# Kernel tuning notes

Hardware: AMD Instinct MI355X
Metric: run time of the kernel (lower is better)

The kernel has to match this reference:

```python
import jax, jax.numpy as jnp
import numpy as np

B, S, D, F, E = 2, 2048, 1024, 4096, 8

def _xavier(key, shape):
    fan_in, fan_out = shape[-2], shape[-1]
    lim = np.sqrt(6.0 / (fan_in + fan_out))
    return jax.random.uniform(key, shape, jnp.float32, -lim, lim)

def setup_inputs() -> dict:
    key = jax.random.key(0)
    kx, k1, k2, kg = jax.random.split(key, 4)
    return {
        "x": jax.random.normal(kx, (B, S, D), jnp.float32),
        "W1": _xavier(k1, (E, D, F)),            # expert linear1 weights
        "b1": jnp.zeros((E, F), jnp.float32),
        "W2": _xavier(k2, (E, F, D)),            # expert linear2 weights
        "b2": jnp.zeros((E, D), jnp.float32),
        "Wg": _xavier(kg, (D, E)),               # gate weight
        "bg": jnp.zeros((E,), jnp.float32),
        "num_experts_per_token": 2,
    }

def reference(x, W1, b1, W2, b2, Wg, bg, num_experts_per_token):
    k = num_experts_per_token
    gate = jnp.einsum('bsd,de->bse', x, Wg) + bg            # [B,S,E]
    top_scores, top_idx = jax.lax.top_k(gate, k)            # [B,S,k]
    probs = jax.nn.softmax(top_scores, axis=-1)             # softmax over top-k only
    # dense combine weights [B,S,E]: scatter top-k probs into expert slots
    comb = jnp.sum(jax.nn.one_hot(top_idx, E, dtype=x.dtype) * probs[..., None], axis=-2)
    # every expert over every token (naive-MoE math, dropout in eval mode)
    h = jax.nn.relu(jnp.einsum('bsd,edf->bsef', x, W1) + b1)   # [B,S,E,F]
    y = jnp.einsum('bsef,efd->bsed', h, W2) + b2               # [B,S,E,D]
    return jnp.einsum('bse,bsed->bsd', comb, y)                # [B,S,D]
```

## Files before the change

kernel.cpp:

```cpp
#include <hip/hip_runtime.h>
#include <hip/hip_bf16.h>

#define TOK  4096
#define DD   1024
#define FF   4096
#define EE   8
#define BM   128
#define BN   128
#define BK   64
#define ASTR 88
#define MPAD (TOK*2 + EE*BM)

typedef __attribute__((ext_vector_type(8))) short  short8;
typedef __attribute__((ext_vector_type(4))) float  f32x4;

__device__ inline unsigned short f2bf(float f) {
    __hip_bfloat16 h = __float2bfloat16(f);
    return __builtin_bit_cast(unsigned short, h);
}

__global__ __launch_bounds__(256) void cvt_x(const float* __restrict__ x,
                                             unsigned short* __restrict__ xb) {
    size_t i = ((size_t)blockIdx.x * 256 + threadIdx.x) * 4;
    float4 v = *(const float4*)(x + i);
    ushort4 o;
    o.x = f2bf(v.x); o.y = f2bf(v.y); o.z = f2bf(v.z); o.w = f2bf(v.w);
    *(ushort4*)(xb + i) = o;
}

__global__ __launch_bounds__(256) void gate_kernel(const float* __restrict__ x,
                                                   const float* __restrict__ Wg,
                                                   const float* __restrict__ bg,
                                                   int* __restrict__ tidx,
                                                   float* __restrict__ tp,
                                                   int* __restrict__ counts) {
    int token = blockIdx.x;
    int t = threadIdx.x;
    const float* xr = x + (size_t)token * DD;
    float acc[EE];
#pragma unroll
    for (int e = 0; e < EE; e++) acc[e] = 0.f;

    float4 xv = *(const float4*)(xr + t * 4);
    const float* wr = Wg + (size_t)(t * 4) * EE;
#pragma unroll
    for (int j = 0; j < 4; j++) {
        float xd = (j == 0) ? xv.x : (j == 1) ? xv.y : (j == 2) ? xv.z : xv.w;
        const float* wj = wr + j * EE;
#pragma unroll
        for (int e = 0; e < EE; e++) acc[e] += xd * wj[e];
    }
#pragma unroll
    for (int e = 0; e < EE; e++) {
        float v = acc[e];
#pragma unroll
        for (int off = 32; off >= 1; off >>= 1) v += __shfl_xor(v, off, 64);
        acc[e] = v;
    }
    __shared__ float sred[4][EE];
    int lane = t & 63, wv = t >> 6;
    if (lane == 0) {
#pragma unroll
        for (int e = 0; e < EE; e++) sred[wv][e] = acc[e];
    }
    __syncthreads();
    if (t == 0) {
        float s[EE];
#pragma unroll
        for (int e = 0; e < EE; e++)
            s[e] = sred[0][e] + sred[1][e] + sred[2][e] + sred[3][e] + bg[e];
        int i0 = 0;
#pragma unroll
        for (int e = 1; e < EE; e++) if (s[e] > s[i0]) i0 = e;
        int i1 = (i0 == 0) ? 1 : 0;
#pragma unroll
        for (int e = 0; e < EE; e++) if (e != i0 && s[e] > s[i1]) i1 = e;
        float e1 = expf(s[i1] - s[i0]);
        float inv = 1.f / (1.f + e1);
        tidx[token * 2]     = i0;
        tidx[token * 2 + 1] = i1;
        tp[token * 2]       = inv;
        tp[token * 2 + 1]   = e1 * inv;
        atomicAdd(&counts[i0], 1);
        atomicAdd(&counts[i1], 1);
    }
}

__global__ void route_offsets(const int* __restrict__ counts,
                              int* __restrict__ offs, int* __restrict__ cursor) {
    if (threadIdx.x == 0) {
        int o = 0; offs[0] = 0;
        for (int e = 0; e < EE; e++) {
            cursor[e] = o;
            o += ((counts[e] + BM - 1) / BM) * BM;
            offs[e + 1] = o;
        }
    }
}

__global__ __launch_bounds__(256) void route_scatter(const int* __restrict__ tidx,
                                                     const float* __restrict__ tp,
                                                     int* __restrict__ cursor,
                                                     int* __restrict__ row_token,
                                                     float* __restrict__ row_prob) {
    int token = blockIdx.x * 256 + threadIdx.x;
    if (token >= TOK) return;
#pragma unroll
    for (int j = 0; j < 2; j++) {
        int e = tidx[token * 2 + j];
        int slot = atomicAdd(&cursor[e], 1);
        row_token[slot] = token;
        row_prob[slot]  = tp[token * 2 + j];
    }
}

__global__ __launch_bounds__(256) void transpose_cvt(const float* __restrict__ src,
                                                     unsigned short* __restrict__ dst,
                                                     int R, int C) {
    __shared__ float tile[64][68];
    int c0 = blockIdx.x * 64, r0 = blockIdx.y * 64;
    size_t slab = (size_t)blockIdx.z * R * C;
    src += slab; dst += slab;
    int t = threadIdx.x;
#pragma unroll
    for (int i = 0; i < 4; i++) {
        int r = i * 16 + (t >> 4);
        int c = (t & 15) * 4;
        float4 v = *(const float4*)(src + (size_t)(r0 + r) * C + c0 + c);
        tile[r][c] = v.x; tile[r][c + 1] = v.y; tile[r][c + 2] = v.z; tile[r][c + 3] = v.w;
    }
    __syncthreads();
#pragma unroll
    for (int i = 0; i < 4; i++) {
        int c = i * 16 + (t >> 4);
        int r = (t & 15) * 4;
        ushort4 o;
        o.x = f2bf(tile[r][c]);     o.y = f2bf(tile[r + 1][c]);
        o.z = f2bf(tile[r + 2][c]); o.w = f2bf(tile[r + 3][c]);
        *(ushort4*)(dst + (size_t)(c0 + c) * R + r0 + r) = o;
    }
}

__global__ __launch_bounds__(256) void ffn1(const unsigned short* __restrict__ xb,
                                            const unsigned short* __restrict__ w1t,
                                            const float* __restrict__ b1,
                                            const int* __restrict__ offs,
                                            const int* __restrict__ row_token,
                                            unsigned short* __restrict__ Hb) {
    int n0 = blockIdx.x * BN, m0 = blockIdx.y * BM;
    int e = 0;
    while (e < EE && m0 >= offs[e + 1]) e++;
    if (e >= EE) return;

    __shared__ unsigned short As[BM * ASTR];
    __shared__ unsigned short Bs[BN * ASTR];
    int t = threadIdx.x, lane = t & 63, wv = t >> 6;
    int wm = (wv >> 1) * 64, wn = (wv & 1) * 64;
    f32x4 acc[4][4];
#pragma unroll
    for (int i = 0; i < 4; i++)
#pragma unroll
        for (int j = 0; j < 4; j++) acc[i][j] = (f32x4){0.f, 0.f, 0.f, 0.f};

    const unsigned short* wb = w1t + (size_t)e * FF * DD;
    int arow[4];
#pragma unroll
    for (int i = 0; i < 4; i++) {
        int tok = row_token[m0 + i * 32 + (t >> 3)];
        arow[i] = (tok < 0) ? 0 : tok;
    }

    for (int kt = 0; kt < DD / BK; ++kt) {
        __syncthreads();
#pragma unroll
        for (int i = 0; i < 4; i++) {
            int r = i * 32 + (t >> 3);
            uint4 va = *(const uint4*)(xb + (size_t)arow[i] * DD + kt * BK + (t & 7) * 8);
            *(uint4*)(&As[r * ASTR + (t & 7) * 8]) = va;
            uint4 vb = *(const uint4*)(wb + (size_t)(n0 + r) * DD + kt * BK + (t & 7) * 8);
            *(uint4*)(&Bs[r * ASTR + (t & 7) * 8]) = vb;
        }
        __syncthreads();
#pragma unroll
        for (int kk = 0; kk < 2; kk++) {
            short8 af[4], bfm[4];
#pragma unroll
            for (int i = 0; i < 4; i++) {
                af[i]  = *(const short8*)(&As[(wm + i * 16 + (lane & 15)) * ASTR + kk * 32 + (lane >> 4) * 8]);
                bfm[i] = *(const short8*)(&Bs[(wn + i * 16 + (lane & 15)) * ASTR + kk * 32 + (lane >> 4) * 8]);
            }
#pragma unroll
            for (int i = 0; i < 4; i++)
#pragma unroll
                for (int j = 0; j < 4; j++)
                    acc[i][j] = __builtin_amdgcn_mfma_f32_16x16x32_bf16(af[i], bfm[j], acc[i][j], 0, 0, 0);
        }
    }
    const float* b1e = b1 + (size_t)e * FF;
#pragma unroll
    for (int j = 0; j < 4; j++) {
        int col = n0 + wn + j * 16 + (lane & 15);
        float bv = b1e[col];
#pragma unroll
        for (int i = 0; i < 4; i++) {
            int rb = m0 + wm + i * 16 + (lane >> 4) * 4;
#pragma unroll
            for (int r = 0; r < 4; r++) {
                float hv = fmaxf(acc[i][j][r] + bv, 0.f);
                Hb[(size_t)(rb + r) * FF + col] = f2bf(hv);
            }
        }
    }
}

__global__ __launch_bounds__(256) void ffn2(const unsigned short* __restrict__ Hb,
                                            const unsigned short* __restrict__ w2t,
                                            const float* __restrict__ b2,
                                            const int* __restrict__ offs,
                                            const int* __restrict__ row_token,
                                            const float* __restrict__ row_prob,
                                            float* __restrict__ out) {
    int n0 = blockIdx.x * BN, m0 = blockIdx.y * BM;
    int e = 0;
    while (e < EE && m0 >= offs[e + 1]) e++;
    if (e >= EE) return;

    __shared__ unsigned short As[BM * ASTR];
    __shared__ unsigned short Bs[BN * ASTR];
    int t = threadIdx.x, lane = t & 63, wv = t >> 6;
    int wm = (wv >> 1) * 64, wn = (wv & 1) * 64;
    f32x4 acc[4][4];
#pragma unroll
    for (int i = 0; i < 4; i++)
#pragma unroll
        for (int j = 0; j < 4; j++) acc[i][j] = (f32x4){0.f, 0.f, 0.f, 0.f};

    const unsigned short* wb = w2t + (size_t)e * DD * FF;

    for (int kt = 0; kt < FF / BK; ++kt) {
        __syncthreads();
#pragma unroll
        for (int i = 0; i < 4; i++) {
            int r = i * 32 + (t >> 3);
            uint4 va = *(const uint4*)(Hb + (size_t)(m0 + r) * FF + kt * BK + (t & 7) * 8);
            *(uint4*)(&As[r * ASTR + (t & 7) * 8]) = va;
            uint4 vb = *(const uint4*)(wb + (size_t)(n0 + r) * FF + kt * BK + (t & 7) * 8);
            *(uint4*)(&Bs[r * ASTR + (t & 7) * 8]) = vb;
        }
        __syncthreads();
#pragma unroll
        for (int kk = 0; kk < 2; kk++) {
            short8 af[4], bfm[4];
#pragma unroll
            for (int i = 0; i < 4; i++) {
                af[i]  = *(const short8*)(&As[(wm + i * 16 + (lane & 15)) * ASTR + kk * 32 + (lane >> 4) * 8]);
                bfm[i] = *(const short8*)(&Bs[(wn + i * 16 + (lane & 15)) * ASTR + kk * 32 + (lane >> 4) * 8]);
            }
#pragma unroll
            for (int i = 0; i < 4; i++)
#pragma unroll
                for (int j = 0; j < 4; j++)
                    acc[i][j] = __builtin_amdgcn_mfma_f32_16x16x32_bf16(af[i], bfm[j], acc[i][j], 0, 0, 0);
        }
    }
    const float* b2e = b2 + (size_t)e * DD;
#pragma unroll
    for (int i = 0; i < 4; i++) {
#pragma unroll
        for (int r = 0; r < 4; r++) {
            int slot = m0 + wm + i * 16 + (lane >> 4) * 4 + r;
            int tok = row_token[slot];
            if (tok < 0) continue;
            float p = row_prob[slot];
            float* orow = out + (size_t)tok * DD;
#pragma unroll
            for (int j = 0; j < 4; j++) {
                int col = n0 + wn + j * 16 + (lane & 15);
                atomicAdd(orow + col, p * (acc[i][j][r] + b2e[col]));
            }
        }
    }
}

extern "C" void kernel_launch(void* const* d_in, const int* in_sizes, int n_in,
                              void* d_out, int out_size, void* d_ws, size_t ws_size,
                              hipStream_t stream) {
    const float* x  = (const float*)d_in[0];
    const float* W1 = (const float*)d_in[1];
    const float* b1 = (const float*)d_in[2];
    const float* W2 = (const float*)d_in[3];
    const float* b2 = (const float*)d_in[4];
    const float* Wg = (const float*)d_in[5];
    const float* bg = (const float*)d_in[6];
    float* out = (float*)d_out;

    char* w = (char*)d_ws;
    unsigned short* xb   = (unsigned short*)w; w += (size_t)TOK * DD * 2;
    unsigned short* W1bt = (unsigned short*)w; w += (size_t)EE * FF * DD * 2;
    unsigned short* W2bt = (unsigned short*)w; w += (size_t)EE * DD * FF * 2;
    unsigned short* Hb   = (unsigned short*)w; w += (size_t)MPAD * FF * 2;
    int*   counts    = (int*)w;  w += 256;
    int*   offs      = (int*)w;  w += 256;
    int*   cursor    = (int*)w;  w += 256;
    int*   row_token = (int*)w;  w += (size_t)MPAD * 4;
    float* row_prob  = (float*)w; w += (size_t)MPAD * 4;
    int*   tidx      = (int*)w;  w += (size_t)TOK * 2 * 4;
    float* tp        = (float*)w; w += (size_t)TOK * 2 * 4;

    hipMemsetAsync(counts, 0, 256, stream);
    hipMemsetAsync(row_token, 0xFF, (size_t)MPAD * 4, stream);
    hipMemsetAsync(out, 0, (size_t)TOK * DD * 4, stream);

    cvt_x<<<(TOK * DD / 4) / 256, 256, 0, stream>>>(x, xb);
    gate_kernel<<<TOK, 256, 0, stream>>>(x, Wg, bg, tidx, tp, counts);
    route_offsets<<<1, 64, 0, stream>>>(counts, offs, cursor);
    route_scatter<<<TOK / 256, 256, 0, stream>>>(tidx, tp, cursor, row_token, row_prob);
    transpose_cvt<<<dim3(FF / 64, DD / 64, EE), 256, 0, stream>>>(W1, W1bt, DD, FF);
    transpose_cvt<<<dim3(DD / 64, FF / 64, EE), 256, 0, stream>>>(W2, W2bt, FF, DD);
    ffn1<<<dim3(FF / BN, MPAD / BM), 256, 0, stream>>>(xb, W1bt, b1, offs, row_token, Hb);
    ffn2<<<dim3(DD / BN, MPAD / BM), 256, 0, stream>>>(Hb, W2bt, b2, offs, row_token, row_prob, out);
}
```

Before: 798.6 us.

## Use direct global-to-LDS loads, swizzled grid, and atomic-free combine

The GEMM kernels now copy tiles straight from global memory into LDS with the global_load_lds builtin instead of staging through registers. The unpadded LDS layout this requires may introduce bank conflicts on the MFMA fragment reads. The 2D grid becomes a 1D grid with an XCD-style swizzle meant to improve L2 locality. ffn2 now writes per-slot outputs to a scratch buffer that reuses the W1 bf16 region, and a new combine kernel does the weighted sum of each token's two expert outputs, replacing float atomics and the output memset. The transpose tile padding also changes from 68 to 65.

```diff
diff --git a/kernel.cpp b/kernel.cpp
--- a/kernel.cpp
+++ b/kernel.cpp
@@ -8,7 +8,6 @@
 #define BM   128
 #define BN   128
 #define BK   64
-#define ASTR 88
 #define MPAD (TOK*2 + EE*BM)
 
 typedef __attribute__((ext_vector_type(8))) short  short8;
@@ -17,6 +16,13 @@
 __device__ inline unsigned short f2bf(float f) {
     __hip_bfloat16 h = __float2bfloat16(f);
     return __builtin_bit_cast(unsigned short, h);
+}
+
+__device__ inline void cp16(void* lds, const void* g) {
+    __builtin_amdgcn_global_load_lds(
+        (const __attribute__((address_space(1))) void*)g,
+        (__attribute__((address_space(3))) void*)lds,
+        16, 0, 0);
 }
 
 __global__ __launch_bounds__(256) void cvt_x(const float* __restrict__ x,
@@ -102,7 +108,8 @@
                                                      const float* __restrict__ tp,
                                                      int* __restrict__ cursor,
                                                      int* __restrict__ row_token,
-                                                     float* __restrict__ row_prob) {
+                                                     float* __restrict__ row_prob,
+                                                     int* __restrict__ slot_of) {
     int token = blockIdx.x * 256 + threadIdx.x;
     if (token >= TOK) return;
 #pragma unroll
@@ -111,13 +118,14 @@
         int slot = atomicAdd(&cursor[e], 1);
         row_token[slot] = token;
         row_prob[slot]  = tp[token * 2 + j];
+        slot_of[token * 2 + j] = slot;
     }
 }
 
 __global__ __launch_bounds__(256) void transpose_cvt(const float* __restrict__ src,
                                                      unsigned short* __restrict__ dst,
                                                      int R, int C) {
-    __shared__ float tile[64][68];
+    __shared__ float tile[64][65];
     int c0 = blockIdx.x * 64, r0 = blockIdx.y * 64;
     size_t slab = (size_t)blockIdx.z * R * C;
     src += slab; dst += slab;
@@ -147,38 +155,43 @@
                                             const int* __restrict__ offs,
                                             const int* __restrict__ row_token,
                                             unsigned short* __restrict__ Hb) {
-    int n0 = blockIdx.x * BN, m0 = blockIdx.y * BM;
+    __shared__ unsigned short As[BM * BK];
+    __shared__ unsigned short Bs[BN * BK];
+    int bid = blockIdx.x, nwg = gridDim.x;
+    int swz = (bid & 7) * (nwg >> 3) + (bid >> 3);
+    int n0 = (swz % (FF / BN)) * BN;
+    int m0 = (swz / (FF / BN)) * BM;
     int e = 0;
     while (e < EE && m0 >= offs[e + 1]) e++;
     if (e >= EE) return;
 
-    __shared__ unsigned short As[BM * ASTR];
-    __shared__ unsigned short Bs[BN * ASTR];
     int t = threadIdx.x, lane = t & 63, wv = t >> 6;
     int wm = (wv >> 1) * 64, wn = (wv & 1) * 64;
+
+    const unsigned short* wb = w1t + (size_t)e * FF * DD;
+
+    const unsigned short* gA[4];
+    const unsigned short* gB[4];
+#pragma unroll
+    for (int i = 0; i < 4; i++) {
+        int row = i * 32 + wv * 8 + (lane >> 3);
+        int tok = row_token[m0 + row];
+        if (tok < 0) tok = 0;
+        gA[i] = xb + (size_t)tok * DD + (lane & 7) * 8;
+        gB[i] = wb + (size_t)(n0 + row) * DD + (lane & 7) * 8;
+    }
+
     f32x4 acc[4][4];
 #pragma unroll
     for (int i = 0; i < 4; i++)
 #pragma unroll
         for (int j = 0; j < 4; j++) acc[i][j] = (f32x4){0.f, 0.f, 0.f, 0.f};
 
-    const unsigned short* wb = w1t + (size_t)e * FF * DD;
-    int arow[4];
-#pragma unroll
-    for (int i = 0; i < 4; i++) {
-        int tok = row_token[m0 + i * 32 + (t >> 3)];
-        arow[i] = (tok < 0) ? 0 : tok;
-    }
-
     for (int kt = 0; kt < DD / BK; ++kt) {
-        __syncthreads();
 #pragma unroll
         for (int i = 0; i < 4; i++) {
-            int r = i * 32 + (t >> 3);
-            uint4 va = *(const uint4*)(xb + (size_t)arow[i] * DD + kt * BK + (t & 7) * 8);
-            *(uint4*)(&As[r * ASTR + (t & 7) * 8]) = va;
-            uint4 vb = *(const uint4*)(wb + (size_t)(n0 + r) * DD + kt * BK + (t & 7) * 8);
-            *(uint4*)(&Bs[r * ASTR + (t & 7) * 8]) = vb;
+            cp16(&As[(i * 32 + wv * 8) * BK], gA[i] + kt * BK);
+            cp16(&Bs[(i * 32 + wv * 8) * BK], gB[i] + kt * BK);
         }
         __syncthreads();
 #pragma unroll
@@ -186,8 +199,8 @@
             short8 af[4], bfm[4];
 #pragma unroll
             for (int i = 0; i < 4; i++) {
-                af[i]  = *(const short8*)(&As[(wm + i * 16 + (lane & 15)) * ASTR + kk * 32 + (lane >> 4) * 8]);
-                bfm[i] = *(const short8*)(&Bs[(wn + i * 16 + (lane & 15)) * ASTR + kk * 32 + (lane >> 4) * 8]);
+                af[i]  = *(const short8*)(&As[(wm + i * 16 + (lane & 15)) * BK + kk * 32 + (lane >> 4) * 8]);
+                bfm[i] = *(const short8*)(&Bs[(wn + i * 16 + (lane & 15)) * BK + kk * 32 + (lane >> 4) * 8]);
             }
 #pragma unroll
             for (int i = 0; i < 4; i++)
@@ -195,6 +208,7 @@
                 for (int j = 0; j < 4; j++)
                     acc[i][j] = __builtin_amdgcn_mfma_f32_16x16x32_bf16(af[i], bfm[j], acc[i][j], 0, 0, 0);
         }
+        __syncthreads();
     }
     const float* b1e = b1 + (size_t)e * FF;
 #pragma unroll
@@ -217,35 +231,42 @@
                                             const unsigned short* __restrict__ w2t,
                                             const float* __restrict__ b2,
                                             const int* __restrict__ offs,
-                                            const int* __restrict__ row_token,
-                                            const float* __restrict__ row_prob,
-                                            float* __restrict__ out) {
-    int n0 = blockIdx.x * BN, m0 = blockIdx.y * BM;
+                                            float* __restrict__ Y) {
+    __shared__ unsigned short As[BM * BK];
+    __shared__ unsigned short Bs[BN * BK];
+    int bid = blockIdx.x, nwg = gridDim.x;
+    int swz = (bid & 7) * (nwg >> 3) + (bid >> 3);
+    int n0 = (swz % (DD / BN)) * BN;
+    int m0 = (swz / (DD / BN)) * BM;
     int e = 0;
     while (e < EE && m0 >= offs[e + 1]) e++;
     if (e >= EE) return;
 
-    __shared__ unsigned short As[BM * ASTR];
-    __shared__ unsigned short Bs[BN * ASTR];
     int t = threadIdx.x, lane = t & 63, wv = t >> 6;
     int wm = (wv >> 1) * 64, wn = (wv & 1) * 64;
+
+    const unsigned short* wb = w2t + (size_t)e * DD * FF;
+
+    const unsigned short* gA[4];
+    const unsigned short* gB[4];
+#pragma unroll
+    for (int i = 0; i < 4; i++) {
+        int row = i * 32 + wv * 8 + (lane >> 3);
+        gA[i] = Hb + (size_t)(m0 + row) * FF + (lane & 7) * 8;
+        gB[i] = wb + (size_t)(n0 + row) * FF + (lane & 7) * 8;
+    }
+
     f32x4 acc[4][4];
 #pragma unroll
     for (int i = 0; i < 4; i++)
 #pragma unroll
         for (int j = 0; j < 4; j++) acc[i][j] = (f32x4){0.f, 0.f, 0.f, 0.f};
 
-    const unsigned short* wb = w2t + (size_t)e * DD * FF;
-
     for (int kt = 0; kt < FF / BK; ++kt) {
-        __syncthreads();
 #pragma unroll
         for (int i = 0; i < 4; i++) {
-            int r = i * 32 + (t >> 3);
-            uint4 va = *(const uint4*)(Hb + (size_t)(m0 + r) * FF + kt * BK + (t & 7) * 8);
-            *(uint4*)(&As[r * ASTR + (t & 7) * 8]) = va;
-            uint4 vb = *(const uint4*)(wb + (size_t)(n0 + r) * FF + kt * BK + (t & 7) * 8);
-            *(uint4*)(&Bs[r * ASTR + (t & 7) * 8]) = vb;
+            cp16(&As[(i * 32 + wv * 8) * BK], gA[i] + kt * BK);
+            cp16(&Bs[(i * 32 + wv * 8) * BK], gB[i] + kt * BK);
         }
         __syncthreads();
 #pragma unroll
@@ -253,8 +274,8 @@
             short8 af[4], bfm[4];
 #pragma unroll
             for (int i = 0; i < 4; i++) {
-                af[i]  = *(const short8*)(&As[(wm + i * 16 + (lane & 15)) * ASTR + kk * 32 + (lane >> 4) * 8]);
-                bfm[i] = *(const short8*)(&Bs[(wn + i * 16 + (lane & 15)) * ASTR + kk * 32 + (lane >> 4) * 8]);
+                af[i]  = *(const short8*)(&As[(wm + i * 16 + (lane & 15)) * BK + kk * 32 + (lane >> 4) * 8]);
+                bfm[i] = *(const short8*)(&Bs[(wn + i * 16 + (lane & 15)) * BK + kk * 32 + (lane >> 4) * 8]);
             }
 #pragma unroll
             for (int i = 0; i < 4; i++)
@@ -262,6 +283,7 @@
                 for (int j = 0; j < 4; j++)
                     acc[i][j] = __builtin_amdgcn_mfma_f32_16x16x32_bf16(af[i], bfm[j], acc[i][j], 0, 0, 0);
         }
+        __syncthreads();
     }
     const float* b2e = b2 + (size_t)e * DD;
 #pragma unroll
@@ -269,17 +291,32 @@
 #pragma unroll
         for (int r = 0; r < 4; r++) {
             int slot = m0 + wm + i * 16 + (lane >> 4) * 4 + r;
-            int tok = row_token[slot];
-            if (tok < 0) continue;
-            float p = row_prob[slot];
-            float* orow = out + (size_t)tok * DD;
+            float* yrow = Y + (size_t)slot * DD;
 #pragma unroll
             for (int j = 0; j < 4; j++) {
                 int col = n0 + wn + j * 16 + (lane & 15);
-                atomicAdd(orow + col, p * (acc[i][j][r] + b2e[col]));
+                yrow[col] = acc[i][j][r] + b2e[col];
             }
         }
     }
+}
+
+__global__ __launch_bounds__(256) void combine(const float* __restrict__ Y,
+                                               const float* __restrict__ tp,
+                                               const int* __restrict__ slot_of,
+                                               float* __restrict__ out) {
+    int tkn = blockIdx.x;
+    int c = threadIdx.x * 4;
+    int s0 = slot_of[tkn * 2], s1 = slot_of[tkn * 2 + 1];
+    float p0 = tp[tkn * 2],    p1 = tp[tkn * 2 + 1];
+    float4 y0 = *(const float4*)(Y + (size_t)s0 * DD + c);
+    float4 y1 = *(const float4*)(Y + (size_t)s1 * DD + c);
+    float4 o;
+    o.x = p0 * y0.x + p1 * y1.x;
+    o.y = p0 * y0.y + p1 * y1.y;
+    o.z = p0 * y0.z + p1 * y1.z;
+    o.w = p0 * y0.w + p1 * y1.w;
+    *(float4*)(out + (size_t)tkn * DD + c) = o;
 }
 
 extern "C" void kernel_launch(void* const* d_in, const int* in_sizes, int n_in,
@@ -306,17 +343,19 @@
     float* row_prob  = (float*)w; w += (size_t)MPAD * 4;
     int*   tidx      = (int*)w;  w += (size_t)TOK * 2 * 4;
     float* tp        = (float*)w; w += (size_t)TOK * 2 * 4;
+    int*   slot_of   = (int*)w;  w += (size_t)TOK * 2 * 4;
+    float* Y = (float*)W1bt;
 
     hipMemsetAsync(counts, 0, 256, stream);
     hipMemsetAsync(row_token, 0xFF, (size_t)MPAD * 4, stream);
-    hipMemsetAsync(out, 0, (size_t)TOK * DD * 4, stream);
 
     cvt_x<<<(TOK * DD / 4) / 256, 256, 0, stream>>>(x, xb);
     gate_kernel<<<TOK, 256, 0, stream>>>(x, Wg, bg, tidx, tp, counts);
     route_offsets<<<1, 64, 0, stream>>>(counts, offs, cursor);
-    route_scatter<<<TOK / 256, 256, 0, stream>>>(tidx, tp, cursor, row_token, row_prob);
+    route_scatter<<<TOK / 256, 256, 0, stream>>>(tidx, tp, cursor, row_token, row_prob, slot_of);
     transpose_cvt<<<dim3(FF / 64, DD / 64, EE), 256, 0, stream>>>(W1, W1bt, DD, FF);
     transpose_cvt<<<dim3(DD / 64, FF / 64, EE), 256, 0, stream>>>(W2, W2bt, FF, DD);
-    ffn1<<<dim3(FF / BN, MPAD / BM), 256, 0, stream>>>(xb, W1bt, b1, offs, row_token, Hb);
-    ffn2<<<dim3(DD / BN, MPAD / BM), 256, 0, stream>>>(Hb, W2bt, b2, offs, row_token, row_prob, out);
-}
+    ffn1<<<(FF / BN) * (MPAD / BM), 256, 0, stream>>>(xb, W1bt, b1, offs, row_token, Hb);
+    ffn2<<<(DD / BN) * (MPAD / BM), 256, 0, stream>>>(Hb, W2bt, b2, offs, Y);
+    combine<<<TOK, 256, 0, stream>>>(Y, tp, slot_of, out);
+}
```

Measured after the change: 728.9 us. -8.7%, faster.
